# Kernel tuning notes

Hardware: AMD Instinct MI355X
Metric: run time of the kernel (lower is better)

Reference implementation:

```python
import jax, jax.numpy as jnp
import numpy as np
from jax import lax

STRIDE = 1
PAD = 0  # circular padding amount; 0 with kernel_size=1
NEG_SLOPE = 0.2


def _tran(t, conv_w, conv_b):
    # Conv2d with padding_mode='circular' (wrap-pad then VALID conv), NCHW/OIHW.
    if PAD > 0:
        t = jnp.pad(t, ((0, 0), (0, 0), (PAD, PAD), (PAD, PAD)), mode='wrap')
    out = lax.conv_general_dilated(
        t, conv_w, window_strides=(STRIDE, STRIDE), padding='VALID',
        dimension_numbers=('NCHW', 'OIHW', 'NCHW'))
    return out + conv_b[None, :, None, None]


def setup_inputs() -> dict:
    key = jax.random.key(0)
    ks = jax.random.split(key, 6)
    B, N_in, C_in, F_in = 16, 2048, 4, 16
    N_out = 2048
    feat_len = 64  # = C*F after conv (kernel=1, stride=1, pad=0 -> 4*16)
    return {
        'x': jax.random.normal(ks[0], (B, N_in, C_in, F_in), jnp.float32),
        'n': jax.random.normal(ks[1], (B, N_in, C_in, F_in), jnp.float32),
        'conv_w': jax.random.normal(ks[2], (N_out, N_in, 1, 1), jnp.float32) * 0.02,
        'conv_b': jax.random.normal(ks[3], (N_out,), jnp.float32) * 0.02,
        'att1_w': jax.random.normal(ks[4], (1, feat_len), jnp.float32) * 0.1,
        'att2_w': jax.random.normal(ks[5], (1, feat_len), jnp.float32) * 0.1,
    }


def reference(x, n, conv_w, conv_b, att1_w, att2_w):
    x = _tran(x, conv_w, conv_b)  # (B, N, C, F)
    n = _tran(n, conv_w, conv_b)
    B, N, C, F = x.shape
    xf = x.reshape(B, N, C * F)  # (B, N, feat)
    nf = n.reshape(B, N, C * F)
    s1 = jnp.einsum('bnf,of->bno', xf, att1_w)  # (B, N, 1)
    s2 = jnp.einsum('bnf,of->bno', nf, att2_w)  # (B, N, 1)
    # a[b, i, j] = s1[b, j] + s2[b, i]
    a = jnp.swapaxes(s1, -1, -2) + s2  # (B, N, N)
    a = jax.nn.leaky_relu(a, NEG_SLOPE)
    a = jax.nn.softmax(a, axis=1)  # NOTE: softmax over dim=1 (rows), as in the torch code
    out = jnp.einsum('bij,bjf->bif', a, xf)  # (B, N, feat)
    return out.reshape(B, N, C, F)
```

## Files before the change

kernel.cpp:

```cpp
#include <hip/hip_runtime.h>
#include <math.h>


#define BB 16
#define NN 2048
#define FEAT 64
#define BM 64
#define BK 32
#define NCH 16
#define CHL 128

typedef __attribute__((ext_vector_type(8))) short short8v;
typedef __attribute__((ext_vector_type(8))) ushort ushort8v;
typedef __attribute__((ext_vector_type(4))) float f32x4;

__device__ __forceinline__ float lrelu(float t) {
    return fmaxf(t, 0.2f * t);
}

__device__ __forceinline__ ushort bf16_rne(float f) {
    unsigned u = __float_as_uint(f);
    unsigned r = u + 0x7FFF + ((u >> 16) & 1);
    return (ushort)(r >> 16);
}
__device__ __forceinline__ float bf16_to_f(ushort h) {
    return __uint_as_float(((unsigned)h) << 16);
}

__device__ __forceinline__ void gl_lds16(const void* g, void* l) {
    __builtin_amdgcn_global_load_lds(
        (const __attribute__((address_space(1))) unsigned int*)g,
        (__attribute__((address_space(3))) unsigned int*)l,
        16, 0, 0);
}

__global__ __launch_bounds__(256) void k_cvtW(
        const float* __restrict__ W, ushort* __restrict__ Wh,
        ushort* __restrict__ Wl) {
    int idx = (blockIdx.x * 256 + threadIdx.x) * 4;
    float4 w = *(const float4*)(W + idx);
    ushort h0 = bf16_rne(w.x), h1 = bf16_rne(w.y),
           h2 = bf16_rne(w.z), h3 = bf16_rne(w.w);
    ushort l0 = bf16_rne(w.x - bf16_to_f(h0)), l1 = bf16_rne(w.y - bf16_to_f(h1)),
           l2 = bf16_rne(w.z - bf16_to_f(h2)), l3 = bf16_rne(w.w - bf16_to_f(h3));
    *(ushort4*)(Wh + idx) = make_ushort4(h0, h1, h2, h3);
    *(ushort4*)(Wl + idx) = make_ushort4(l0, l1, l2, l3);
}

__global__ __launch_bounds__(256) void k_cvtX(
        const float* __restrict__ x, ushort* __restrict__ xh,
        ushort* __restrict__ xl) {
    __shared__ float tile[64][65];
    const int k0 = blockIdx.x * 64, b = blockIdx.y, t = threadIdx.x;
#pragma unroll
    for (int i = 0; i < 4; ++i) {
        int row = (t >> 4) + i * 16, c4 = (t & 15) * 4;
        *(float4*)&tile[row][c4] =
            *(const float4*)(x + ((size_t)b * NN + k0 + row) * FEAT + c4);
    }
    __syncthreads();
    const int f = t >> 2, kg = t & 3;
    ushort hi[16], lo[16];
#pragma unroll
    for (int e = 0; e < 16; ++e) {
        float v = tile[kg * 16 + e][f];
        ushort h = bf16_rne(v);
        hi[e] = h;
        lo[e] = bf16_rne(v - bf16_to_f(h));
    }
    size_t base = ((size_t)b * FEAT + f) * NN + k0 + kg * 16;
#pragma unroll
    for (int q = 0; q < 2; ++q) {
        ushort8v vh, vl;
#pragma unroll
        for (int e = 0; e < 8; ++e) { vh[e] = hi[q * 8 + e]; vl[e] = lo[q * 8 + e]; }
        *(ushort8v*)(xh + base + q * 8) = vh;
        *(ushort8v*)(xl + base + q * 8) = vl;
    }
}

__device__ __forceinline__ void stage_tile(
        const ushort* __restrict__ Wh, const ushort* __restrict__ Wl,
        const ushort* __restrict__ xh, const ushort* __restrict__ xl,
        int wrow0, int xrow0, int k0, char* ldsbuf, int wave, int lane) {
    const int rc = lane >> 3;
    const int kk = ((lane & 7) ^ rc) << 3;
#pragma unroll
    for (int q = 0; q < 2; ++q) {
        const int c = wave * 2 + q;
        const size_t wr = (size_t)(wrow0 + c * 8 + rc) * NN + k0 + kk;
        const size_t xr = (size_t)(xrow0 + c * 8 + rc) * NN + k0 + kk;
        char* ldc = ldsbuf + c * 1024;
        gl_lds16(Wh + wr, ldc);
        gl_lds16(Wl + wr, ldc + 8192);
        gl_lds16(xh + xr, ldc + 16384);
        gl_lds16(xl + xr, ldc + 24576);
    }
}

#define COMPUTE_TILE(BUF)                                                     \
    {                                                                         \
        const char* bp = (BUF);                                               \
        _Pragma("unroll")                                                     \
        for (int s = 0; s < 2; ++s) {                                         \
            const int kslot = s * 4 + kq;                                     \
            int rowA0 = wr + col, rowA1 = wr + 16 + col;                      \
            int offA0 = (rowA0 * 128 + kslot * 16) ^ ((rowA0 & 7) << 4);      \
            int offA1 = (rowA1 * 128 + kslot * 16) ^ ((rowA1 & 7) << 4);      \
            short8v Ah0 = *(const short8v*)(bp + offA0);                      \
            short8v Ah1 = *(const short8v*)(bp + offA1);                      \
            short8v Al0 = *(const short8v*)(bp + 8192 + offA0);               \
            short8v Al1 = *(const short8v*)(bp + 8192 + offA1);               \
            int fB0 = wc + col, fB1 = wc + 16 + col;                          \
            int offB0 = (fB0 * 128 + kslot * 16) ^ ((fB0 & 7) << 4);          \
            int offB1 = (fB1 * 128 + kslot * 16) ^ ((fB1 & 7) << 4);          \
            short8v Bh0 = *(const short8v*)(bp + 16384 + offB0);              \
            short8v Bh1 = *(const short8v*)(bp + 16384 + offB1);              \
            short8v Bl0 = *(const short8v*)(bp + 24576 + offB0);              \
            short8v Bl1 = *(const short8v*)(bp + 24576 + offB1);              \
            a00 = __builtin_amdgcn_mfma_f32_16x16x32_bf16(Ah0, Bh0, a00, 0, 0, 0); \
            a00 = __builtin_amdgcn_mfma_f32_16x16x32_bf16(Ah0, Bl0, a00, 0, 0, 0); \
            a00 = __builtin_amdgcn_mfma_f32_16x16x32_bf16(Al0, Bh0, a00, 0, 0, 0); \
            a01 = __builtin_amdgcn_mfma_f32_16x16x32_bf16(Ah0, Bh1, a01, 0, 0, 0); \
            a01 = __builtin_amdgcn_mfma_f32_16x16x32_bf16(Ah0, Bl1, a01, 0, 0, 0); \
            a01 = __builtin_amdgcn_mfma_f32_16x16x32_bf16(Al0, Bh1, a01, 0, 0, 0); \
            a10 = __builtin_amdgcn_mfma_f32_16x16x32_bf16(Ah1, Bh0, a10, 0, 0, 0); \
            a10 = __builtin_amdgcn_mfma_f32_16x16x32_bf16(Ah1, Bl0, a10, 0, 0, 0); \
            a10 = __builtin_amdgcn_mfma_f32_16x16x32_bf16(Al1, Bh0, a10, 0, 0, 0); \
            a11 = __builtin_amdgcn_mfma_f32_16x16x32_bf16(Ah1, Bh1, a11, 0, 0, 0); \
            a11 = __builtin_amdgcn_mfma_f32_16x16x32_bf16(Ah1, Bl1, a11, 0, 0, 0); \
            a11 = __builtin_amdgcn_mfma_f32_16x16x32_bf16(Al1, Bh1, a11, 0, 0, 0); \
        }                                                                     \
    }

__global__ __launch_bounds__(256, 2) void k1_mfma2(
        const ushort* __restrict__ Wh, const ushort* __restrict__ Wl,
        const ushort* __restrict__ xh, const ushort* __restrict__ xl,
        const float* __restrict__ bias, float* __restrict__ xf) {
    __shared__ __align__(16) char lds[65536];
    const int bid = blockIdx.x;
    const int xcd = bid & 7, j = bid >> 3;
    const int b   = xcd * 2 + (j & 1);
    const int rt0 = (j >> 1) * 64;
    const int t = threadIdx.x, wave = t >> 6, lane = t & 63;
    const int wr = (wave >> 1) * 32, wc = (wave & 1) * 32;
    const int col = lane & 15, kq = lane >> 4;
    const int xrow0 = b * FEAT;

    f32x4 a00 = {}, a01 = {}, a10 = {}, a11 = {};

    stage_tile(Wh, Wl, xh, xl, rt0, xrow0, 0, lds, wave, lane);
    for (int kt = 0; kt < 31; ++kt) {
        stage_tile(Wh, Wl, xh, xl, rt0, xrow0, (kt + 1) * 64,
                   lds + ((kt + 1) & 1) * 32768, wave, lane);
        asm volatile("s_waitcnt vmcnt(8)" ::: "memory");
        __builtin_amdgcn_s_barrier();
        COMPUTE_TILE(lds + (kt & 1) * 32768);
        asm volatile("s_waitcnt lgkmcnt(0)" ::: "memory");
        __builtin_amdgcn_s_barrier();
    }
    asm volatile("s_waitcnt vmcnt(0)" ::: "memory");
    __builtin_amdgcn_s_barrier();
    COMPUTE_TILE(lds + 32768);

    const size_t obase = (size_t)b * NN + rt0;
#pragma unroll
    for (int r = 0; r < 4; ++r) {
        const int oA = wr + kq * 4 + r;
        const int oB = oA + 16;
        const float bA = bias[rt0 + oA], bB = bias[rt0 + oB];
        xf[(obase + oA) * FEAT + wc + col]      = a00[r] + bA;
        xf[(obase + oA) * FEAT + wc + 16 + col] = a01[r] + bA;
        xf[(obase + oB) * FEAT + wc + col]      = a10[r] + bB;
        xf[(obase + oB) * FEAT + wc + 16 + col] = a11[r] + bB;
    }
}

__global__ __launch_bounds__(256) void k1_conv(
        const float* __restrict__ x, const float* __restrict__ W,
        const float* __restrict__ bias, float* __restrict__ xf) {
    __shared__ float Ws[BK][BM + 4];
    __shared__ float Xs[BK][FEAT];
    const int o0 = blockIdx.x * BM;
    const int b  = blockIdx.y;
    const int t  = threadIdx.x;
    const int ty = t >> 4, tx = t & 15;
    float acc[4][4] = {};
    for (int k0 = 0; k0 < NN; k0 += BK) {
#pragma unroll
        for (int r = 0; r < 2; ++r) {
            int v = t + r * 256;
            int m = v >> 3, k = (v & 7) * 4;
            float4 w4 = *(const float4*)(W + (size_t)(o0 + m) * NN + k0 + k);
            Ws[k + 0][m] = w4.x; Ws[k + 1][m] = w4.y;
            Ws[k + 2][m] = w4.z; Ws[k + 3][m] = w4.w;
        }
#pragma unroll
        for (int r = 0; r < 2; ++r) {
            int v = t + r * 256;
            int k = v >> 4, hw = (v & 15) * 4;
            *(float4*)&Xs[k][hw] =
                *(const float4*)(x + ((size_t)b * NN + k0 + k) * FEAT + hw);
        }
        __syncthreads();
#pragma unroll
        for (int kk = 0; kk < BK; ++kk) {
            float a[4], c[4];
            *(float4*)a = *(const float4*)&Ws[kk][ty * 4];
            *(float4*)c = *(const float4*)&Xs[kk][tx * 4];
#pragma unroll
            for (int ii = 0; ii < 4; ++ii)
#pragma unroll
                for (int ff = 0; ff < 4; ++ff)
                    acc[ii][ff] += a[ii] * c[ff];
        }
        __syncthreads();
    }
#pragma unroll
    for (int ii = 0; ii < 4; ++ii) {
        int o = o0 + ty * 4 + ii;
        float bv = bias[o];
        float4 r = make_float4(acc[ii][0] + bv, acc[ii][1] + bv,
                               acc[ii][2] + bv, acc[ii][3] + bv);
        *(float4*)(xf + ((size_t)b * NN + o) * FEAT + tx * 4) = r;
    }
}

__global__ __launch_bounds__(256) void k0_ntilde(
        const float* __restrict__ n, const float* __restrict__ att2,
        float* __restrict__ nt) {
    int t = blockIdx.x * 256 + threadIdx.x;
    int b = t >> 11, i = t & (NN - 1);
    const float4* row = (const float4*)(n + ((size_t)b * NN + i) * FEAT);
    const float4* a2  = (const float4*)att2;
    float s = 0.f;
#pragma unroll
    for (int q = 0; q < 16; ++q) {
        float4 v = row[q], w = a2[q];
        s += v.x * w.x + v.y * w.y + v.z * w.z + v.w * w.w;
    }
    nt[i * BB + b] = s;
}

__global__ __launch_bounds__(256) void k2_s2(
        const float* __restrict__ W, const float* __restrict__ nt,
        const float* __restrict__ bias, const float* __restrict__ att2,
        float* __restrict__ s2) {
    int t = blockIdx.x * 256 + threadIdx.x;
    int o = t >> 4, b = t & 15;
    float acc = 0.f;
    for (int i = 0; i < NN; i += 4) {
        float4 w4 = *(const float4*)(W + (size_t)o * NN + i);
        acc += w4.x * nt[(i + 0) * BB + b] + w4.y * nt[(i + 1) * BB + b]
             + w4.z * nt[(i + 2) * BB + b] + w4.w * nt[(i + 3) * BB + b];
    }
    float A2 = 0.f;
#pragma unroll
    for (int q = 0; q < FEAT; ++q) A2 += att2[q];
    s2[(size_t)b * NN + o] = acc + bias[o] * A2;
}

__global__ __launch_bounds__(256) void k2b_s1(
        const float* __restrict__ xf, const float* __restrict__ att1,
        float* __restrict__ s1) {
    int t = blockIdx.x * 256 + threadIdx.x;
    const float4* row = (const float4*)(xf + (size_t)t * FEAT);
    const float4* a1  = (const float4*)att1;
    float s = 0.f;
#pragma unroll
    for (int q = 0; q < 16; ++q) {
        float4 v = row[q], w = a1[q];
        s += v.x * w.x + v.y * w.y + v.z * w.z + v.w * w.w;
    }
    s1[t] = s;
}

__device__ __forceinline__ void scan2048(float* buf, int t) {
    for (int off = 1; off < 2048; off <<= 1) {
        int i0 = t, i1 = t + 1024;
        float x0 = (i0 >= off) ? buf[i0 - off] : 0.f;
        float c0 = buf[i0];
        float x1 = (i1 >= off) ? buf[i1 - off] : 0.f;
        float c1 = buf[i1];
        __syncthreads();
        buf[i0] = c0 + x0;
        buf[i1] = c1 + x1;
        __syncthreads();
    }
}

__global__ __launch_bounds__(1024) void ksort(
        const float* __restrict__ s1, const float* __restrict__ s2,
        float* __restrict__ s1s, int* __restrict__ p1,
        float* __restrict__ s2s, float* __restrict__ E1suf,
        float* __restrict__ E2) {
    __shared__ float key[2048];
    __shared__ int   val[2048];
    __shared__ float buf[2048];
    const int b = blockIdx.y, arr = blockIdx.x, t = threadIdx.x;
    const float* src = (arr == 0 ? s1 : s2) + (size_t)b * NN;
    key[t] = src[t]; key[t + 1024] = src[t + 1024];
    val[t] = t;      val[t + 1024] = t + 1024;
    __syncthreads();
    for (int k = 2; k <= 2048; k <<= 1) {
        for (int j = k >> 1; j > 0; j >>= 1) {
#pragma unroll
            for (int r = 0; r < 2; ++r) {
                int i = r * 1024 + t;
                int l = i ^ j;
                if (l > i) {
                    bool up = ((i & k) == 0);
                    float ki = key[i], kl = key[l];
                    if (up ? (ki > kl) : (ki < kl)) {
                        key[i] = kl; key[l] = ki;
                        int vi = val[i]; val[i] = val[l]; val[l] = vi;
                    }
                }
            }
            __syncthreads();
        }
    }
    const size_t base = (size_t)b * NN;
    if (arr == 0) {
        s1s[base + t] = key[t]; s1s[base + t + 1024] = key[t + 1024];
        p1[base + t]  = val[t]; p1[base + t + 1024]  = val[t + 1024];
    } else {
        s2s[base + t] = key[t]; s2s[base + t + 1024] = key[t + 1024];
        buf[t] = __expf(0.2f * key[t]);
        buf[t + 1024] = __expf(0.2f * key[t + 1024]);
        __syncthreads();
        scan2048(buf, t);
        E2[base + t] = buf[t]; E2[base + t + 1024] = buf[t + 1024];
        __syncthreads();
        buf[t] = __expf(key[2047 - t]);
        buf[t + 1024] = __expf(key[2047 - (t + 1024)]);
        __syncthreads();
        scan2048(buf, t);
        E1suf[base + 2047 - t] = buf[t];
        E1suf[base + 2047 - (t + 1024)] = buf[t + 1024];
    }
}

__global__ __launch_bounds__(256) void k_ab(
        const float* __restrict__ s1s, const float* __restrict__ s2s,
        const float* __restrict__ E1suf, const float* __restrict__ E2,
        float* __restrict__ as, float* __restrict__ bs) {
    int idx = blockIdx.x * 256 + threadIdx.x;
    int b = idx >> 11;
    const size_t base = (size_t)b * NN;
    float s1v = s1s[idx];
    float thr = -s1v;
    const float* S2 = s2s + base;
    int lo = 0, hi = NN;
    while (lo < hi) { int mid = (lo + hi) >> 1; if (S2[mid] < thr) lo = mid + 1; else hi = mid; }
    float e1 = (lo < NN) ? E1suf[base + lo] : 0.f;
    float e2 = (lo > 0)  ? E2[base + lo - 1] : 0.f;
    float ea = __expf(s1v), eb = __expf(0.2f * s1v);
    float zi = 1.0f / (ea * e1 + eb * e2);
    as[idx] = ea * zi;
    bs[idx] = eb * zi;
}

__global__ __launch_bounds__(64) void kscanA(
        const int* __restrict__ p1, const float* __restrict__ as,
        const float* __restrict__ bs, const float* __restrict__ xf,
        float* __restrict__ CTA, float* __restrict__ CTB) {
    const int b = blockIdx.y, c = blockIdx.x, f = threadIdx.x;
    const size_t base = (size_t)b * NN;
    float sA = 0.f, sB = 0.f;
#pragma unroll 8
    for (int r = 0; r < CHL; ++r) {
        int t = c * CHL + r;
        int j = p1[base + t];
        float xv = xf[(base + j) * FEAT + f];
        sA += as[base + t] * xv;
        sB += bs[base + t] * xv;
    }
    CTA[((size_t)b * NCH + c) * FEAT + f] = sA;
    CTB[((size_t)b * NCH + c) * FEAT + f] = sB;
}

__global__ __launch_bounds__(64) void kscanB(
        const int* __restrict__ p1, const float* __restrict__ as,
        const float* __restrict__ bs, const float* __restrict__ xf,
        const float* __restrict__ CTA, const float* __restrict__ CTB,
        float* __restrict__ PA, float* __restrict__ PB) {
    const int b = blockIdx.y, c = blockIdx.x, f = threadIdx.x;
    const size_t base = (size_t)b * NN;
    float offA = 0.f, offB = 0.f;
    for (int cc = 0; cc < NCH; ++cc) {
        float av = CTA[((size_t)b * NCH + cc) * FEAT + f];
        float bv = CTB[((size_t)b * NCH + cc) * FEAT + f];
        if (cc > c) offA += av;
        if (cc < c) offB += bv;
    }
    float run = offB;
#pragma unroll 4
    for (int r = 0; r < CHL; ++r) {
        int t = c * CHL + r;
        int j = p1[base + t];
        float xv = xf[(base + j) * FEAT + f];
        run += bs[base + t] * xv;
        PB[(base + t) * FEAT + f] = run;
    }
    run = offA;
#pragma unroll 4
    for (int r = CHL - 1; r >= 0; --r) {
        int t = c * CHL + r;
        int j = p1[base + t];
        float xv = xf[(base + j) * FEAT + f];
        run += as[base + t] * xv;
        PA[(base + t) * FEAT + f] = run;
    }
}

__global__ __launch_bounds__(256) void k4_sep(
        const float* __restrict__ s2, const float* __restrict__ s1s,
        const float* __restrict__ PA, const float* __restrict__ PB,
        float* __restrict__ out) {
    const int b = blockIdx.y;
    const int i = blockIdx.x * 16 + (threadIdx.x >> 4);
    const int fg = threadIdx.x & 15;
    const size_t base = (size_t)b * NN;
    float s2v = s2[base + i];
    float thr = -s2v;
    const float* S1 = s1s + base;
    int lo = 0, hi = NN;
    while (lo < hi) { int mid = (lo + hi) >> 1; if (S1[mid] < thr) lo = mid + 1; else hi = mid; }
    float eA = __expf(s2v), eB = __expf(0.2f * s2v);
    float4 pa = make_float4(0.f, 0.f, 0.f, 0.f);
    float4 pb = make_float4(0.f, 0.f, 0.f, 0.f);
    if (lo < NN) pa = *(const float4*)(PA + (base + lo) * FEAT + fg * 4);
    if (lo > 0)  pb = *(const float4*)(PB + (base + lo - 1) * FEAT + fg * 4);
    float4 o;
    o.x = eA * pa.x + eB * pb.x;
    o.y = eA * pa.y + eB * pb.y;
    o.z = eA * pa.z + eB * pb.z;
    o.w = eA * pa.w + eB * pb.w;
    *(float4*)(out + (base + i) * FEAT + fg * 4) = o;
}

extern "C" void kernel_launch(void* const* d_in, const int* in_sizes, int n_in,
                              void* d_out, int out_size, void* d_ws, size_t ws_size,
                              hipStream_t stream) {
    const float* x      = (const float*)d_in[0];
    const float* n      = (const float*)d_in[1];
    const float* conv_w = (const float*)d_in[2];
    const float* conv_b = (const float*)d_in[3];
    const float* att1   = (const float*)d_in[4];
    const float* att2   = (const float*)d_in[5];
    float* outp = (float*)d_out;
    float* xf = outp;

    float* ws    = (float*)d_ws;
    float* s1    = ws;
    float* s2    = s1    + (size_t)BB * NN;
    float* nt    = s2    + (size_t)BB * NN;
    float* s1s   = nt    + (size_t)BB * NN;
    int*   p1    = (int*)(s1s + (size_t)BB * NN);
    float* s2s   = (float*)p1 + (size_t)BB * NN;
    float* E1suf = s2s   + (size_t)BB * NN;
    float* E2    = E1suf + (size_t)BB * NN;
    float* as    = E2    + (size_t)BB * NN;
    float* bs    = as    + (size_t)BB * NN;
    float* CTA   = bs    + (size_t)BB * NN;
    float* CTB   = CTA   + (size_t)BB * NCH * FEAT;
    float* PA    = CTB   + (size_t)BB * NCH * FEAT;
    float* PB    = PA    + (size_t)BB * NN * FEAT;
    ushort* Wh   = (ushort*)PA;
    ushort* Wl   = Wh + (size_t)NN * NN;
    ushort* xh   = (ushort*)(PB + (size_t)BB * NN * FEAT);
    ushort* xl   = xh + (size_t)BB * NN * FEAT;

    const size_t need_mfma =
        (size_t)((char*)(xl + (size_t)BB * NN * FEAT) - (char*)d_ws);
    const bool use_mfma = ws_size >= need_mfma;

    k0_ntilde<<<dim3(BB * NN / 256), dim3(256), 0, stream>>>(n, att2, nt);
    if (use_mfma) {
        k_cvtW<<<dim3(NN * NN / 1024), dim3(256), 0, stream>>>(conv_w, Wh, Wl);
        k_cvtX<<<dim3(NN / 64, BB), dim3(256), 0, stream>>>(x, xh, xl);
        k1_mfma2<<<dim3(512), dim3(256), 0, stream>>>(Wh, Wl, xh, xl,
                                                      conv_b, xf);
    } else {
        k1_conv<<<dim3(NN / BM, BB), dim3(256), 0, stream>>>(x, conv_w, conv_b, xf);
    }
    k2_s2<<<dim3(NN * BB / 256), dim3(256), 0, stream>>>(conv_w, nt, conv_b, att2, s2);
    k2b_s1<<<dim3(BB * NN / 256), dim3(256), 0, stream>>>(xf, att1, s1);
    ksort<<<dim3(2, BB), dim3(1024), 0, stream>>>(s1, s2, s1s, p1, s2s, E1suf, E2);
    k_ab<<<dim3(BB * NN / 256), dim3(256), 0, stream>>>(s1s, s2s, E1suf, E2, as, bs);
    kscanA<<<dim3(NCH, BB), dim3(64), 0, stream>>>(p1, as, bs, xf, CTA, CTB);
    kscanB<<<dim3(NCH, BB), dim3(64), 0, stream>>>(p1, as, bs, xf, CTA, CTB, PA, PB);
    k4_sep<<<dim3(NN / 16, BB), dim3(256), 0, stream>>>(s2, s1s, PA, PB, outp);
}
```

Before: 252.1 us.

## Fold s2 projection into MFMA conv as extra batch rows

The s2 = W·ñ matvec is moved from a separate fp32 kernel into the MFMA conv kernel. The ñ vectors are written in split bf16 hi/lo form by k0_ntilde and laid out as an extra 17th batch slot in the x buffers, and 32 extra blocks are launched. This removes the k2_s2 pass, which re-read the full 16 MB fp32 weight matrix, at the cost of some wasted MFMA work on padded columns. It also changes the workspace layout.

Result: faster. 217.6 us (-13.7%).

```diff
diff --git a/kernel.cpp b/kernel.cpp
--- a/kernel.cpp
+++ b/kernel.cpp
@@ -76,6 +76,28 @@
         for (int e = 0; e < 8; ++e) { vh[e] = hi[q * 8 + e]; vl[e] = lo[q * 8 + e]; }
         *(ushort8v*)(xh + base + q * 8) = vh;
         *(ushort8v*)(xl + base + q * 8) = vl;
+    }
+}
+
+__global__ __launch_bounds__(256) void k0_ntilde(
+        const float* __restrict__ n, const float* __restrict__ att2,
+        float* __restrict__ nt, ushort* __restrict__ nth,
+        ushort* __restrict__ ntl, int wbf) {
+    int t = blockIdx.x * 256 + threadIdx.x;
+    int b = t >> 11, i = t & (NN - 1);
+    const float4* row = (const float4*)(n + ((size_t)b * NN + i) * FEAT);
+    const float4* a2  = (const float4*)att2;
+    float s = 0.f;
+#pragma unroll
+    for (int q = 0; q < 16; ++q) {
+        float4 v = row[q], w = a2[q];
+        s += v.x * w.x + v.y * w.y + v.z * w.z + v.w * w.w;
+    }
+    nt[i * BB + b] = s;
+    if (wbf) {
+        ushort h = bf16_rne(s);
+        nth[(size_t)b * NN + i] = h;
+        ntl[(size_t)b * NN + i] = bf16_rne(s - bf16_to_f(h));
     }
 }
 
@@ -136,12 +158,19 @@
 __global__ __launch_bounds__(256, 2) void k1_mfma2(
         const ushort* __restrict__ Wh, const ushort* __restrict__ Wl,
         const ushort* __restrict__ xh, const ushort* __restrict__ xl,
-        const float* __restrict__ bias, float* __restrict__ xf) {
+        const float* __restrict__ bias, const float* __restrict__ att2,
+        float* __restrict__ xf, float* __restrict__ s2out) {
     __shared__ __align__(16) char lds[65536];
     const int bid = blockIdx.x;
-    const int xcd = bid & 7, j = bid >> 3;
-    const int b   = xcd * 2 + (j & 1);
-    const int rt0 = (j >> 1) * 64;
+    int b, rt0;
+    if (bid < 512) {
+        const int xcd = bid & 7, j = bid >> 3;
+        b   = xcd * 2 + (j & 1);
+        rt0 = (j >> 1) * 64;
+    } else {
+        b   = 16;
+        rt0 = (bid - 512) * 64;
+    }
     const int t = threadIdx.x, wave = t >> 6, lane = t & 63;
     const int wr = (wave >> 1) * 32, wc = (wave & 1) * 32;
     const int col = lane & 15, kq = lane >> 4;
@@ -163,16 +192,33 @@
     __builtin_amdgcn_s_barrier();
     COMPUTE_TILE(lds + 32768);
 
-    const size_t obase = (size_t)b * NN + rt0;
-#pragma unroll
-    for (int r = 0; r < 4; ++r) {
-        const int oA = wr + kq * 4 + r;
-        const int oB = oA + 16;
-        const float bA = bias[rt0 + oA], bB = bias[rt0 + oB];
-        xf[(obase + oA) * FEAT + wc + col]      = a00[r] + bA;
-        xf[(obase + oA) * FEAT + wc + 16 + col] = a01[r] + bA;
-        xf[(obase + oB) * FEAT + wc + col]      = a10[r] + bB;
-        xf[(obase + oB) * FEAT + wc + 16 + col] = a11[r] + bB;
+    if (b < 16) {
+        const size_t obase = (size_t)b * NN + rt0;
+#pragma unroll
+        for (int r = 0; r < 4; ++r) {
+            const int oA = wr + kq * 4 + r;
+            const int oB = oA + 16;
+            const float bA = bias[rt0 + oA], bB = bias[rt0 + oB];
+            xf[(obase + oA) * FEAT + wc + col]      = a00[r] + bA;
+            xf[(obase + oA) * FEAT + wc + 16 + col] = a01[r] + bA;
+            xf[(obase + oB) * FEAT + wc + col]      = a10[r] + bB;
+            xf[(obase + oB) * FEAT + wc + 16 + col] = a11[r] + bB;
+        }
+    } else if (wc == 0) {
+        float A2 = 0.f;
+        const float4* a2 = (const float4*)att2;
+#pragma unroll
+        for (int q = 0; q < 16; ++q) {
+            float4 v = a2[q];
+            A2 += v.x + v.y + v.z + v.w;
+        }
+#pragma unroll
+        for (int r = 0; r < 4; ++r) {
+            const int oA = wr + kq * 4 + r;
+            const int oB = oA + 16;
+            s2out[(size_t)col * NN + rt0 + oA] = a00[r] + bias[rt0 + oA] * A2;
+            s2out[(size_t)col * NN + rt0 + oB] = a10[r] + bias[rt0 + oB] * A2;
+        }
     }
 }
 
@@ -224,22 +270,6 @@
                                acc[ii][2] + bv, acc[ii][3] + bv);
         *(float4*)(xf + ((size_t)b * NN + o) * FEAT + tx * 4) = r;
     }
-}
-
-__global__ __launch_bounds__(256) void k0_ntilde(
-        const float* __restrict__ n, const float* __restrict__ att2,
-        float* __restrict__ nt) {
-    int t = blockIdx.x * 256 + threadIdx.x;
-    int b = t >> 11, i = t & (NN - 1);
-    const float4* row = (const float4*)(n + ((size_t)b * NN + i) * FEAT);
-    const float4* a2  = (const float4*)att2;
-    float s = 0.f;
-#pragma unroll
-    for (int q = 0; q < 16; ++q) {
-        float4 v = row[q], w = a2[q];
-        s += v.x * w.x + v.y * w.y + v.z * w.z + v.w * w.w;
-    }
-    nt[i * BB + b] = s;
 }
 
 __global__ __launch_bounds__(256) void k2_s2(
@@ -465,27 +495,31 @@
     float* bs    = as    + (size_t)BB * NN;
     float* CTA   = bs    + (size_t)BB * NN;
     float* CTB   = CTA   + (size_t)BB * NCH * FEAT;
-    float* PA    = CTB   + (size_t)BB * NCH * FEAT;
-    float* PB    = PA    + (size_t)BB * NN * FEAT;
+    ushort* xh   = (ushort*)(CTB + (size_t)BB * NCH * FEAT);
+    ushort* nth  = xh + (size_t)1024 * NN;
+    ushort* xl   = xh + (size_t)1040 * NN;
+    ushort* ntl  = xl + (size_t)1024 * NN;
+    float* PA    = (float*)(xl + (size_t)1040 * NN);
+    float* PB    = PA + (size_t)BB * NN * FEAT;
     ushort* Wh   = (ushort*)PA;
     ushort* Wl   = Wh + (size_t)NN * NN;
-    ushort* xh   = (ushort*)(PB + (size_t)BB * NN * FEAT);
-    ushort* xl   = xh + (size_t)BB * NN * FEAT;
 
     const size_t need_mfma =
-        (size_t)((char*)(xl + (size_t)BB * NN * FEAT) - (char*)d_ws);
+        (size_t)((char*)(PB + (size_t)BB * NN * FEAT) - (char*)d_ws);
     const bool use_mfma = ws_size >= need_mfma;
 
-    k0_ntilde<<<dim3(BB * NN / 256), dim3(256), 0, stream>>>(n, att2, nt);
+    k0_ntilde<<<dim3(BB * NN / 256), dim3(256), 0, stream>>>(
+        n, att2, nt, nth, ntl, use_mfma ? 1 : 0);
     if (use_mfma) {
         k_cvtW<<<dim3(NN * NN / 1024), dim3(256), 0, stream>>>(conv_w, Wh, Wl);
         k_cvtX<<<dim3(NN / 64, BB), dim3(256), 0, stream>>>(x, xh, xl);
-        k1_mfma2<<<dim3(512), dim3(256), 0, stream>>>(Wh, Wl, xh, xl,
-                                                      conv_b, xf);
+        k1_mfma2<<<dim3(544), dim3(256), 0, stream>>>(Wh, Wl, xh, xl,
+                                                      conv_b, att2, xf, s2);
     } else {
         k1_conv<<<dim3(NN / BM, BB), dim3(256), 0, stream>>>(x, conv_w, conv_b, xf);
-    }
-    k2_s2<<<dim3(NN * BB / 256), dim3(256), 0, stream>>>(conv_w, nt, conv_b, att2, s2);
+        k2_s2<<<dim3(NN * BB / 256), dim3(256), 0, stream>>>(conv_w, nt, conv_b,
+                                                             att2, s2);
+    }
     k2b_s1<<<dim3(BB * NN / 256), dim3(256), 0, stream>>>(xf, att1, s1);
     ksort<<<dim3(2, BB), dim3(1024), 0, stream>>>(s1, s2, s1s, p1, s2s, E1suf, E2);
     k_ab<<<dim3(BB * NN / 256), dim3(256), 0, stream>>>(s1s, s2s, E1suf, E2, as, bs);
```
